# Performance work log

Hardware: AMD Instinct MI355X
Metric: run time of the kernel (lower is better)

Reference implementation:

```python
import math
import jax, jax.numpy as jnp
import numpy as np

# Delta lookup table: TAB[rot%8, case] -> (dx, dy)
# case 0: i0==1, case 1: i0==-1, case 2: i1==1 (i0 not +-1), case 3: i1==-1, case 4: none
_TAB = np.zeros((8, 5, 2), dtype=np.int32)
_TAB[0, :4] = [(1, 0), (-1, 0), (0, -1), (0, 1)]
_TAB[1, :4] = [(1, 1), (-1, -1), (1, -1), (-1, 1)]
_TAB[2, :4] = [(0, 1), (0, -1), (1, 0), (-1, 0)]
_TAB[3, :4] = [(-1, 1), (1, -1), (1, 1), (-1, -1)]
_TAB[4, :4] = [(-1, 0), (1, 0), (0, 1), (0, -1)]
_TAB[5, :4] = [(-1, -1), (1, 1), (-1, 1), (1, -1)]
_TAB[6, :4] = [(0, -1), (0, 1), (-1, 0), (1, 0)]
_TAB[7, :4] = [(1, -1), (-1, 1), (-1, -1), (1, 1)]
TAB = jnp.asarray(_TAB)

B, L, D = 16, 4096, 2048


def setup_inputs() -> dict:
    key = jax.random.key(0)
    kx, km, kr = jax.random.split(key, 3)
    x = jax.random.normal(kx, (B, L, D), dtype=jnp.float32)
    move = jax.random.randint(km, (L, 2), -1, 2, dtype=jnp.int32)
    rot = jax.random.randint(kr, (L, 1), 0, 8, dtype=jnp.int32)
    action = jnp.concatenate([move, rot], axis=1)  # [L, 3]
    div_term = jnp.exp(jnp.arange(D, 0, -2, dtype=jnp.float32) * (-math.log(1000.0) / D))  # [D//2]
    return {"x": x, "action": action, "div_term": div_term}


def _positional_encoding(action, div_term, d_model):
    i0, i1, rot = action[:, 0], action[:, 1], action[:, 2] % 8
    # Resolve the elif chain into a case index per step.
    case = jnp.where(i0 == 1, 0,
           jnp.where(i0 == -1, 1,
           jnp.where(i1 == 1, 2,
           jnp.where(i1 == -1, 3, 4))))
    delta = TAB[rot, case]                       # [L, 2]
    counts = jnp.cumsum(delta, axis=0).astype(div_term.dtype)  # [L, 2] cumulative (x_count, y_count)
    phase_x = counts[:, 0:1] * div_term[None, :]  # [L, D//2]
    phase_y = counts[:, 1:2] * div_term[None, :]
    # Interleave: even cols sin(x_count*div), odd cols cos(y_count*div)
    pe = jnp.stack([jnp.sin(phase_x), jnp.cos(phase_y)], axis=-1).reshape(action.shape[0], d_model)
    return pe


def reference(x, action, div_term):
    pe = _positional_encoding(action, div_term, x.shape[-1])  # [L, D]
    return x + pe
```

## Files before the change

### kernel.cpp

```cpp
#include <hip/hip_runtime.h>


#define B_  16
#define L_  4096
#define D_  2048
#define D4_ (D_ / 4)

typedef float f32x4 __attribute__((ext_vector_type(4)));

__constant__ int c_TAB[8][5][2] = {
    { { 1,  0}, {-1,  0}, { 0, -1}, { 0,  1}, {0, 0} },
    { { 1,  1}, {-1, -1}, { 1, -1}, {-1,  1}, {0, 0} },
    { { 0,  1}, { 0, -1}, { 1,  0}, {-1,  0}, {0, 0} },
    { {-1,  1}, { 1, -1}, { 1,  1}, {-1, -1}, {0, 0} },
    { {-1,  0}, { 1,  0}, { 0,  1}, { 0, -1}, {0, 0} },
    { {-1, -1}, { 1,  1}, {-1,  1}, { 1, -1}, {0, 0} },
    { { 0, -1}, { 0,  1}, {-1,  0}, { 1,  0}, {0, 0} },
    { { 1, -1}, {-1,  1}, {-1, -1}, { 1,  1}, {0, 0} },
};

__global__ __launch_bounds__(256) void scan_kernel(
    const int* __restrict__ action,
    float2* __restrict__ counts)
{
    constexpr int NT = 256;
    constexpr int CHUNK = L_ / NT;
    __shared__ int2 sums[NT];

    const int t = threadIdx.x;
    const int base = t * CHUNK;

    int dx[CHUNK], dy[CHUNK];
    int sx = 0, sy = 0;
    #pragma unroll
    for (int j = 0; j < CHUNK; ++j) {
        const int l  = base + j;
        const int i0 = action[l * 3 + 0];
        const int i1 = action[l * 3 + 1];
        int r        = action[l * 3 + 2];
        r = ((r % 8) + 8) % 8;
        const int c = (i0 == 1) ? 0
                    : (i0 == -1) ? 1
                    : (i1 == 1) ? 2
                    : (i1 == -1) ? 3 : 4;
        sx += c_TAB[r][c][0];
        sy += c_TAB[r][c][1];
        dx[j] = sx;
        dy[j] = sy;
    }
    sums[t] = make_int2(sx, sy);
    __syncthreads();

    for (int off = 1; off < NT; off <<= 1) {
        int2 v   = sums[t];
        int2 add = (t >= off) ? sums[t - off] : make_int2(0, 0);
        __syncthreads();
        sums[t] = make_int2(v.x + add.x, v.y + add.y);
        __syncthreads();
    }

    const int px = (t > 0) ? sums[t - 1].x : 0;
    const int py = (t > 0) ? sums[t - 1].y : 0;
    #pragma unroll
    for (int j = 0; j < CHUNK; ++j) {
        counts[base + j] = make_float2((float)(px + dx[j]), (float)(py + dy[j]));
    }
}

__global__ __launch_bounds__(256) void pe_add_kernel(
    const float* __restrict__ x,
    const float2* __restrict__ counts,
    const float2* __restrict__ div2,
    float* __restrict__ out)
{
    const int tid = blockIdx.x * blockDim.x + threadIdx.x;
    const int d4  = tid & (D4_ - 1);
    const int l   = tid >> 9;

    const float2 c  = counts[l];
    const float2 dt = div2[d4];

    f32x4 pe;
    pe.x = sinf(c.x * dt.x);
    pe.y = cosf(c.y * dt.x);
    pe.z = sinf(c.x * dt.y);
    pe.w = cosf(c.y * dt.y);

    const f32x4* __restrict__ xp = (const f32x4*)x + tid;
    f32x4* __restrict__       op = (f32x4*)out + tid;
    constexpr size_t stride4 = (size_t)L_ * D_ / 4;

    #pragma unroll
    for (int g = 0; g < 2; ++g) {
        f32x4 v[8];
        #pragma unroll
        for (int j = 0; j < 8; ++j) {
            v[j] = __builtin_nontemporal_load(xp + (size_t)(g * 8 + j) * stride4);
        }
        #pragma unroll
        for (int j = 0; j < 8; ++j) {
            f32x4 ov = v[j] + pe;
            __builtin_nontemporal_store(ov, op + (size_t)(g * 8 + j) * stride4);
        }
    }
}

extern "C" void kernel_launch(void* const* d_in, const int* in_sizes, int n_in,
                              void* d_out, int out_size, void* d_ws, size_t ws_size,
                              hipStream_t stream) {
    const float* x        = (const float*)d_in[0];
    const int*   action   = (const int*)d_in[1];
    const float* div_term = (const float*)d_in[2];
    float*       out      = (float*)d_out;
    float2*      counts   = (float2*)d_ws;

    scan_kernel<<<1, 256, 0, stream>>>(action, counts);

    const int total4 = (L_ * D_) / 4;
    pe_add_kernel<<<total4 / 256, 256, 0, stream>>>(
        x, counts, (const float2*)div_term, out);
}
```

Measured before the change: 865.2 us.

## Split PE computation into a workspace table and a streaming add kernel

```diff
diff --git a/kernel.cpp b/kernel.cpp
--- a/kernel.cpp
+++ b/kernel.cpp
@@ -67,6 +67,48 @@
     }
 }
 
+__global__ __launch_bounds__(256) void pe_fill_kernel(
+    const float2* __restrict__ counts,
+    const float2* __restrict__ div2,
+    f32x4* __restrict__ pe)
+{
+    const int tid = blockIdx.x * blockDim.x + threadIdx.x;
+    const int d4  = tid & (D4_ - 1);
+    const int l   = tid >> 9;
+
+    const float2 c  = counts[l];
+    const float2 dt = div2[d4];
+
+    f32x4 v;
+    v.x = sinf(c.x * dt.x);
+    v.y = cosf(c.y * dt.x);
+    v.z = sinf(c.x * dt.y);
+    v.w = cosf(c.y * dt.y);
+    pe[tid] = v;
+}
+
+__global__ __launch_bounds__(256) void add_kernel(
+    const f32x4* __restrict__ x,
+    const f32x4* __restrict__ pe,
+    f32x4* __restrict__ out)
+{
+    constexpr size_t STRIDE = (size_t)1 << 22;
+    constexpr size_t PEMASK = ((size_t)1 << 21) - 1;
+    const size_t tid = (size_t)blockIdx.x * blockDim.x + threadIdx.x;
+
+    const f32x4 p = pe[tid & PEMASK];
+
+    f32x4 v[8];
+    #pragma unroll
+    for (int j = 0; j < 8; ++j) {
+        v[j] = x[tid + (size_t)j * STRIDE];
+    }
+    #pragma unroll
+    for (int j = 0; j < 8; ++j) {
+        out[tid + (size_t)j * STRIDE] = v[j] + p;
+    }
+}
+
 __global__ __launch_bounds__(256) void pe_add_kernel(
     const float* __restrict__ x,
     const float2* __restrict__ counts,
@@ -112,11 +154,25 @@
     const int*   action   = (const int*)d_in[1];
     const float* div_term = (const float*)d_in[2];
     float*       out      = (float*)d_out;
-    float2*      counts   = (float2*)d_ws;
+
+    float2* counts = (float2*)d_ws;
+    const size_t PE_OFF   = 32768;
+    const size_t PE_BYTES = (size_t)L_ * D_ * 4;
+    f32x4*  pe     = (f32x4*)((char*)d_ws + PE_OFF);
 
     scan_kernel<<<1, 256, 0, stream>>>(action, counts);
 
-    const int total4 = (L_ * D_) / 4;
-    pe_add_kernel<<<total4 / 256, 256, 0, stream>>>(
-        x, counts, (const float2*)div_term, out);
+    if (ws_size >= PE_OFF + PE_BYTES) {
+        const int peQuads = (L_ * D_) / 4;
+        pe_fill_kernel<<<peQuads / 256, 256, 0, stream>>>(
+            counts, (const float2*)div_term, pe);
+
+        const int addThreads = (B_ * L_ * D_ / 4) / 8;
+        add_kernel<<<addThreads / 256, 256, 0, stream>>>(
+            (const f32x4*)x, pe, (f32x4*)out);
+    } else {
+        const int total4 = (L_ * D_) / 4;
+        pe_add_kernel<<<total4 / 256, 256, 0, stream>>>(
+            x, counts, (const float2*)div_term, out);
+    }
 }
```

New measurement: 901.8 us. +4.2%, slower.
